# Kernel optimization log

Measured on AMD Instinct MI355X. Metric: run time of the kernel, lower is better.

Reference implementation:

```python
import jax, jax.numpy as jnp
import numpy as np

EMBED_DIM = 1024
NUM_HEADS = 16
HEAD_DIM = EMBED_DIM // NUM_HEADS
SCALE = HEAD_DIM ** -0.5
B, S = 4, 2048


def setup_inputs() -> dict:
    key = jax.random.key(0)
    ks = jax.random.split(key, 11)
    std = EMBED_DIM ** -0.5
    return {
        "query": jax.random.normal(ks[0], (B, S, EMBED_DIM), jnp.float32),
        "key": jax.random.normal(ks[1], (B, S, EMBED_DIM), jnp.float32),
        "value": jax.random.normal(ks[2], (B, S, EMBED_DIM), jnp.float32),
        "Wq": jax.random.normal(ks[3], (EMBED_DIM, EMBED_DIM), jnp.float32) * std,
        "bq": jax.random.normal(ks[4], (EMBED_DIM,), jnp.float32) * 0.01,
        "Wk": jax.random.normal(ks[5], (EMBED_DIM, EMBED_DIM), jnp.float32) * std,
        "bk": jax.random.normal(ks[6], (EMBED_DIM,), jnp.float32) * 0.01,
        "Wv": jax.random.normal(ks[7], (EMBED_DIM, EMBED_DIM), jnp.float32) * std,
        "bv": jax.random.normal(ks[8], (EMBED_DIM,), jnp.float32) * 0.01,
        "Wo": jax.random.normal(ks[9], (EMBED_DIM, EMBED_DIM), jnp.float32) * std,
        "bo": jax.random.normal(ks[10], (EMBED_DIM,), jnp.float32) * 0.01,
    }


def reference(query, key, value, Wq, bq, Wk, bk, Wv, bv, Wo, bo):
    b, s, _ = query.shape
    # torch.nn.Linear: x @ W.T + b
    q = query @ Wq.T + bq
    k = key @ Wk.T + bk
    v = value @ Wv.T + bv
    # [b, h, s, d]
    q = q.reshape(b, s, NUM_HEADS, HEAD_DIM).transpose(0, 2, 1, 3)
    k = k.reshape(b, s, NUM_HEADS, HEAD_DIM).transpose(0, 2, 1, 3)
    v = v.reshape(b, s, NUM_HEADS, HEAD_DIM).transpose(0, 2, 1, 3)
    # explicit scores [b, h, s, s]
    scores = jnp.einsum("bhqd,bhkd->bhqk", q, k) * SCALE
    causal = jnp.tril(jnp.ones((s, s), dtype=bool))  # is_causal=True
    scores = jnp.where(causal, scores, -jnp.inf)
    attn = jax.nn.softmax(scores, axis=-1)
    out = jnp.einsum("bhqk,bhkd->bhqd", attn, v)
    out = out.transpose(0, 2, 1, 3).reshape(b, s, EMBED_DIM)
    return out @ Wo.T + bo
```

## Files before the change

kernel.cpp:

```cpp
#include <hip/hip_runtime.h>


#define E 1024
#define HEADS 16
#define HD 64
#define SEQ 2048
#define BATCH 4
#define MROWS (BATCH * SEQ)

typedef __bf16 bf16x8 __attribute__((ext_vector_type(8)));
typedef __bf16 bf16x2 __attribute__((ext_vector_type(2)));
typedef float f32x4 __attribute__((ext_vector_type(4)));
typedef unsigned short ushort8v __attribute__((ext_vector_type(8)));

typedef __attribute__((address_space(1))) void gvoid;
typedef __attribute__((address_space(3))) void lvoid;

__device__ __forceinline__ void async16(const void* g, void* l) {
  __builtin_amdgcn_global_load_lds((gvoid*)g, (lvoid*)l, 16, 0, 0);
}

__device__ __forceinline__ unsigned short f2bf(float f) {
  union { float f; unsigned int u; } v;
  v.f = f;
  unsigned int r = v.u + 0x7FFFu + ((v.u >> 16) & 1u);
  return (unsigned short)(r >> 16);
}

__device__ __forceinline__ unsigned packbf(float a, float b) {
  bf16x2 t;
  t[0] = (__bf16)a;
  t[1] = (__bf16)b;
  return __builtin_bit_cast(unsigned, t);
}

__device__ __forceinline__ void store_out(unsigned short* p, float v) { *p = f2bf(v); }
__device__ __forceinline__ void store_out(float* p, float v) { *p = v; }

struct CastArgs {
  const float* src[4];
  unsigned short* dst[4];
  int n;
};

__global__ __launch_bounds__(256) void cast_kernel(CastArgs a) {
  const float* s = a.src[blockIdx.z];
  unsigned short* d = a.dst[blockIdx.z];
  const int n = a.n;
  const int stride = gridDim.x * blockDim.x * 4;
  for (int i = (blockIdx.x * blockDim.x + threadIdx.x) * 4; i < n; i += stride) {
    float4 v = *(const float4*)(s + i);
    ushort4 o;
    o.x = f2bf(v.x); o.y = f2bf(v.y); o.z = f2bf(v.z); o.w = f2bf(v.w);
    *(ushort4*)(d + i) = o;
  }
}

template <typename OutT>
__device__ __forceinline__ void gemm_body(const unsigned short* __restrict__ A,
                                          const unsigned short* __restrict__ W,
                                          const float* __restrict__ bias,
                                          OutT* __restrict__ out, float scale) {
  __shared__ unsigned short At[128 * 64];
  __shared__ unsigned short Wt[128 * 64];
  const int tid = threadIdx.x;
  const int lane = tid & 63;
  const int wv = tid >> 6;
  const int wm = wv & 1, wn = wv >> 1;
  const int li = lane & 15, g = lane >> 4;
  const int m0 = blockIdx.x * 128, n0 = blockIdx.y * 128;
  f32x4 acc[4][4] = {};

  for (int k0 = 0; k0 < E; k0 += 64) {
    __syncthreads();
#pragma unroll
    for (int i = 0; i < 4; ++i) {
      int c = tid + 256 * i;
      int row = c >> 3, slot = c & 7;
      int gc = slot ^ (row & 7);
      async16(A + (size_t)(m0 + row) * E + k0 + gc * 8, &At[c * 8]);
      async16(W + (size_t)(n0 + row) * E + k0 + gc * 8, &Wt[c * 8]);
    }
    asm volatile("s_waitcnt vmcnt(0)" ::: "memory");
    __syncthreads();
#pragma unroll
    for (int kk = 0; kk < 2; ++kk) {
      bf16x8 af[4], bfr[4];
#pragma unroll
      for (int mt = 0; mt < 4; ++mt) {
        int r = wm * 64 + mt * 16 + li;
        int slot = (kk * 4 + g) ^ (r & 7);
        af[mt] = *(const bf16x8*)&At[r * 64 + slot * 8];
      }
#pragma unroll
      for (int nt = 0; nt < 4; ++nt) {
        int r = wn * 64 + nt * 16 + li;
        int slot = (kk * 4 + g) ^ (r & 7);
        bfr[nt] = *(const bf16x8*)&Wt[r * 64 + slot * 8];
      }
#pragma unroll
      for (int mt = 0; mt < 4; ++mt)
#pragma unroll
        for (int nt = 0; nt < 4; ++nt)
          acc[mt][nt] =
              __builtin_amdgcn_mfma_f32_16x16x32_bf16(af[mt], bfr[nt], acc[mt][nt], 0, 0, 0);
    }
  }

#pragma unroll
  for (int nt = 0; nt < 4; ++nt) {
    int col = n0 + wn * 64 + nt * 16 + li;
    float bv = bias[col];
#pragma unroll
    for (int mt = 0; mt < 4; ++mt) {
#pragma unroll
      for (int r = 0; r < 4; ++r) {
        int row = m0 + wm * 64 + mt * 16 + g * 4 + r;
        store_out(&out[(size_t)row * E + col], (acc[mt][nt][r] + bv) * scale);
      }
    }
  }
}

struct QkvArgs {
  const unsigned short* A[3];
  const unsigned short* W[3];
  const float* bias[3];
  unsigned short* out[3];
  float scale[3];
};

__global__ __launch_bounds__(256) void gemm_qkv(QkvArgs p) {
  const int z = blockIdx.z;
  gemm_body<unsigned short>(p.A[z], p.W[z], p.bias[z], p.out[z], p.scale[z]);
}

__global__ __launch_bounds__(256) void gemm_out_k(const unsigned short* __restrict__ A,
                                                  const unsigned short* __restrict__ W,
                                                  const float* __restrict__ bias,
                                                  float* __restrict__ out) {
  gemm_body<float>(A, W, bias, out, 1.0f);
}

__global__ __launch_bounds__(256, 2) void flash_kernel(const unsigned short* __restrict__ Qb,
                                                       const unsigned short* __restrict__ Kb,
                                                       const unsigned short* __restrict__ Vb,
                                                       unsigned short* __restrict__ Ob) {
  __shared__ unsigned short Kt[2][128 * 64];
  __shared__ unsigned short Vt[2][64 * 128];
  const int p = blockIdx.x;
  const int bh = blockIdx.y;
  const int b = bh >> 4, h16 = bh & 15;
  const size_t base = (size_t)b * SEQ * E + (size_t)h16 * HD;
  const unsigned short* Qp = Qb + base;
  const unsigned short* Kp = Kb + base;
  const unsigned short* Vp = Vb + base;
  unsigned short* Op = Ob + base;
  const int tid = threadIdx.x, lane = tid & 63, wv = tid >> 6;
  const int li = lane & 15, g = lane >> 4;
  const int qlo = p, qhi = 15 - p;
  const int slo = ((g & 1) << 5) | li;

  bf16x8 qfL[2][2], qfH[2][2];
#pragma unroll
  for (int mt = 0; mt < 2; ++mt)
#pragma unroll
    for (int kk = 0; kk < 2; ++kk) {
      int rl = qlo * 128 + wv * 32 + mt * 16 + li;
      int rh = qhi * 128 + wv * 32 + mt * 16 + li;
      qfL[mt][kk] = *(const bf16x8*)(Qp + (size_t)rl * E + kk * 32 + g * 8);
      qfH[mt][kk] = *(const bf16x8*)(Qp + (size_t)rh * E + kk * 32 + g * 8);
    }

  f32x4 oaL[4][2] = {}, oaH[4][2] = {};
  float miL[2] = {-1e30f, -1e30f}, lsL[2] = {0.0f, 0.0f};
  float miH[2] = {-1e30f, -1e30f}, lsH[2] = {0.0f, 0.0f};

  ushort8v vv[4];

  auto loadV = [&](int j) {
#pragma unroll
    for (int i = 0; i < 4; ++i) {
      int c = tid + 256 * i;
      int key = c & 127, db = (c >> 7) * 8;
      vv[i] = *(const ushort8v*)(Vp + (size_t)(j * 128 + key) * E + db);
    }
  };
  auto stageK = [&](int j, int buf) {
#pragma unroll
    for (int i = 0; i < 4; ++i) {
      int c = tid + 256 * i;
      int row = c >> 3, slot = c & 7;
      int gc = slot ^ (row & 7);
      async16(Kp + (size_t)(j * 128 + row) * E + gc * 8, &Kt[buf][c * 8]);
    }
  };
  auto scatV = [&](int buf) {
#pragma unroll
    for (int i = 0; i < 4; ++i) {
      int c = tid + 256 * i;
      int key = c & 127, db = (c >> 7) * 8;
#pragma unroll
      for (int jj = 0; jj < 8; ++jj) {
        int n = db + jj;
        int slot = (key >> 3) ^ (n & 15);
        Vt[buf][n * 128 + slot * 8 + (key & 7)] = vv[i][jj];
      }
    }
  };

  auto compute = [&](const bf16x8 (&qf)[2][2], float (&mi)[2], float (&ls)[2],
                     f32x4 (&oa)[4][2], bool diag, int buf) {
#pragma unroll
    for (int h = 0; h < 2; ++h) {
      if (diag && h * 64 > wv * 32 + 31) continue;

      f32x4 sacc[4][2] = {};
#pragma unroll
      for (int kk = 0; kk < 2; ++kk) {
        bf16x8 kf[4];
#pragma unroll
        for (int nt = 0; nt < 4; ++nt) {
          int key = h * 64 + nt * 16 + li;
          int slot = (kk * 4 + g) ^ (key & 7);
          kf[nt] = *(const bf16x8*)&Kt[buf][key * 64 + slot * 8];
        }
#pragma unroll
        for (int nt = 0; nt < 4; ++nt)
#pragma unroll
          for (int mt = 0; mt < 2; ++mt)
            sacc[nt][mt] =
                __builtin_amdgcn_mfma_f32_16x16x32_bf16(kf[nt], qf[mt][kk], sacc[nt][mt], 0, 0, 0);
      }

      if (diag && h * 64 + 63 > wv * 32) {
#pragma unroll
        for (int nt = 0; nt < 4; ++nt)
#pragma unroll
          for (int mt = 0; mt < 2; ++mt)
#pragma unroll
            for (int r = 0; r < 4; ++r) {
              int keyg = h * 64 + nt * 16 + g * 4 + r;
              int qg = wv * 32 + mt * 16 + li;
              sacc[nt][mt][r] = (keyg > qg) ? -1e30f : sacc[nt][mt][r];
            }
      }

      float alpha[2];
#pragma unroll
      for (int mt = 0; mt < 2; ++mt) {
        float mx = sacc[0][mt][0];
#pragma unroll
        for (int nt = 0; nt < 4; ++nt)
#pragma unroll
          for (int r = 0; r < 4; ++r) mx = fmaxf(mx, sacc[nt][mt][r]);
        mx = fmaxf(mx, __shfl_xor(mx, 16));
        mx = fmaxf(mx, __shfl_xor(mx, 32));
        float mnew = fmaxf(mi[mt], mx);
        alpha[mt] = __expf(mi[mt] - mnew);
        mi[mt] = mnew;
      }

      unsigned pk[4][2][2];
      float rs[2] = {0.0f, 0.0f};
#pragma unroll
      for (int nt = 0; nt < 4; ++nt)
#pragma unroll
        for (int mt = 0; mt < 2; ++mt) {
          float p0 = __expf(sacc[nt][mt][0] - mi[mt]);
          float p1 = __expf(sacc[nt][mt][1] - mi[mt]);
          float p2 = __expf(sacc[nt][mt][2] - mi[mt]);
          float p3 = __expf(sacc[nt][mt][3] - mi[mt]);
          rs[mt] += (p0 + p1) + (p2 + p3);
          pk[nt][mt][0] = packbf(p0, p1);
          pk[nt][mt][1] = packbf(p2, p3);
        }
#pragma unroll
      for (int mt = 0; mt < 2; ++mt) {
        float s = rs[mt];
        s += __shfl_xor(s, 16);
        s += __shfl_xor(s, 32);
        ls[mt] = ls[mt] * alpha[mt] + s;
#pragma unroll
        for (int dt = 0; dt < 4; ++dt) oa[dt][mt] *= alpha[mt];
      }

#pragma unroll
      for (int kk2 = 0; kk2 < 2; ++kk2) {
        const int kc = h * 2 + kk2;
        bf16x8 vf[4];
#pragma unroll
        for (int dt = 0; dt < 4; ++dt) {
          int d = dt * 16 + li;
          int slot = (kc * 4 + g) ^ (d & 15);
          vf[dt] = *(const bf16x8*)&Vt[buf][d * 128 + slot * 8];
        }
#pragma unroll
        for (int mt = 0; mt < 2; ++mt) {
          int a0 = __shfl((int)pk[kk2 * 2][mt][0], slo);
          int a1 = __shfl((int)pk[kk2 * 2][mt][1], slo);
          int a2 = __shfl((int)pk[kk2 * 2][mt][0], slo + 16);
          int a3 = __shfl((int)pk[kk2 * 2][mt][1], slo + 16);
          int c0 = __shfl((int)pk[kk2 * 2 + 1][mt][0], slo);
          int c1 = __shfl((int)pk[kk2 * 2 + 1][mt][1], slo);
          int c2 = __shfl((int)pk[kk2 * 2 + 1][mt][0], slo + 16);
          int c3 = __shfl((int)pk[kk2 * 2 + 1][mt][1], slo + 16);
          bool hi = (g & 2) != 0;
          uint4 bb;
          bb.x = hi ? c0 : a0;
          bb.y = hi ? c1 : a1;
          bb.z = hi ? c2 : a2;
          bb.w = hi ? c3 : a3;
          bf16x8 pf = __builtin_bit_cast(bf16x8, bb);
#pragma unroll
          for (int dt = 0; dt < 4; ++dt)
            oa[dt][mt] =
                __builtin_amdgcn_mfma_f32_16x16x32_bf16(vf[dt], pf, oa[dt][mt], 0, 0, 0);
        }
      }
    }
  };

  loadV(0);
  stageK(0, 0);
  scatV(0);

  for (int j = 0; j <= qhi; ++j) {
    const int buf = j & 1;
    asm volatile("s_waitcnt vmcnt(0)" ::: "memory");
    __syncthreads();
    if (j < qhi) {
      loadV(j + 1);
      stageK(j + 1, buf ^ 1);
    }
    compute(qfH, miH, lsH, oaH, j == qhi, buf);
    if (j <= qlo) compute(qfL, miL, lsL, oaL, j == qlo, buf);
    if (j < qhi) scatV(buf ^ 1);
  }

#pragma unroll
  for (int t = 0; t < 2; ++t) {
    const int qt = t ? qhi : qlo;
    f32x4(&oa)[4][2] = t ? oaH : oaL;
    float* ls = t ? lsH : lsL;
#pragma unroll
    for (int mt = 0; mt < 2; ++mt) {
      float inv = 1.0f / ls[mt];
      int row = qt * 128 + wv * 32 + mt * 16 + li;
#pragma unroll
      for (int dt = 0; dt < 4; ++dt) {
        ushort4 w;
        w.x = f2bf(oa[dt][mt][0] * inv);
        w.y = f2bf(oa[dt][mt][1] * inv);
        w.z = f2bf(oa[dt][mt][2] * inv);
        w.w = f2bf(oa[dt][mt][3] * inv);
        *(ushort4*)(Op + (size_t)row * E + dt * 16 + g * 4) = w;
      }
    }
  }
}

extern "C" void kernel_launch(void* const* d_in, const int* in_sizes, int n_in,
                              void* d_out, int out_size, void* d_ws, size_t ws_size,
                              hipStream_t stream) {
  const float* q  = (const float*)d_in[0];
  const float* k  = (const float*)d_in[1];
  const float* v  = (const float*)d_in[2];
  const float* Wq = (const float*)d_in[3];
  const float* bq = (const float*)d_in[4];
  const float* Wk = (const float*)d_in[5];
  const float* bk = (const float*)d_in[6];
  const float* Wv = (const float*)d_in[7];
  const float* bv = (const float*)d_in[8];
  const float* Wo = (const float*)d_in[9];
  const float* bo = (const float*)d_in[10];

  unsigned short* Xq  = (unsigned short*)d_ws;
  unsigned short* Xk  = Xq + (size_t)MROWS * E;
  unsigned short* Xv  = Xk + (size_t)MROWS * E;
  unsigned short* Wqb = Xv + (size_t)MROWS * E;
  unsigned short* Wkb = Wqb + (size_t)E * E;
  unsigned short* Wvb = Wkb + (size_t)E * E;
  unsigned short* Wob = Wvb + (size_t)E * E;
  unsigned short* Qb  = Wob + (size_t)E * E;
  unsigned short* Kb  = Qb + (size_t)MROWS * E;
  unsigned short* Vb  = Kb + (size_t)MROWS * E;
  unsigned short* Og  = Xq;

  CastArgs ca;
  ca.src[0] = q; ca.src[1] = k; ca.src[2] = v; ca.src[3] = nullptr;
  ca.dst[0] = Xq; ca.dst[1] = Xk; ca.dst[2] = Xv; ca.dst[3] = nullptr;
  ca.n = MROWS * E;
  cast_kernel<<<dim3(1024, 1, 3), 256, 0, stream>>>(ca);

  CastArgs cw;
  cw.src[0] = Wq; cw.src[1] = Wk; cw.src[2] = Wv; cw.src[3] = Wo;
  cw.dst[0] = Wqb; cw.dst[1] = Wkb; cw.dst[2] = Wvb; cw.dst[3] = Wob;
  cw.n = E * E;
  cast_kernel<<<dim3(256, 1, 4), 256, 0, stream>>>(cw);

  QkvArgs p;
  p.A[0] = Xq;  p.A[1] = Xk;  p.A[2] = Xv;
  p.W[0] = Wqb; p.W[1] = Wkb; p.W[2] = Wvb;
  p.bias[0] = bq; p.bias[1] = bk; p.bias[2] = bv;
  p.out[0] = Qb; p.out[1] = Kb; p.out[2] = Vb;
  p.scale[0] = 0.125f; p.scale[1] = 1.0f; p.scale[2] = 1.0f;
  gemm_qkv<<<dim3(64, 8, 3), 256, 0, stream>>>(p);

  flash_kernel<<<dim3(8, 64), 256, 0, stream>>>(Qb, Kb, Vb, Og);

  gemm_out_k<<<dim3(64, 8), 256, 0, stream>>>(Og, Wob, bo, (float*)d_out);
}
```

Before: 405.7 us.

## Single-buffer V tile, use 16x16x16 MFMA for PV without shuffles, merge casts

The PV product now uses the 16x16x16 bf16 MFMA, so the packed probability fragments feed the instruction directly and the per-tile cross-lane shuffles go away. V goes from a double buffer to a single LDS buffer, scattered at the start of each iteration behind an extra barrier, which cuts LDS use and allows launch bounds of 3 blocks per CU. The two cast launches are merged into one 7-slice launch, and bf16 packing switches to the manual rounding helper. In exchange, the V transpose scatter no longer overlaps compute, there is an extra __syncthreads per iteration, and twice as many MFMA instructions are issued for the PV product.

```diff
diff --git a/kernel.cpp b/kernel.cpp
--- a/kernel.cpp
+++ b/kernel.cpp
@@ -9,8 +9,8 @@
 #define MROWS (BATCH * SEQ)
 
 typedef __bf16 bf16x8 __attribute__((ext_vector_type(8)));
-typedef __bf16 bf16x2 __attribute__((ext_vector_type(2)));
 typedef float f32x4 __attribute__((ext_vector_type(4)));
+typedef short s16x4 __attribute__((ext_vector_type(4)));
 typedef unsigned short ushort8v __attribute__((ext_vector_type(8)));
 
 typedef __attribute__((address_space(1))) void gvoid;
@@ -27,26 +27,19 @@
   return (unsigned short)(r >> 16);
 }
 
-__device__ __forceinline__ unsigned packbf(float a, float b) {
-  bf16x2 t;
-  t[0] = (__bf16)a;
-  t[1] = (__bf16)b;
-  return __builtin_bit_cast(unsigned, t);
-}
-
 __device__ __forceinline__ void store_out(unsigned short* p, float v) { *p = f2bf(v); }
 __device__ __forceinline__ void store_out(float* p, float v) { *p = v; }
 
 struct CastArgs {
-  const float* src[4];
-  unsigned short* dst[4];
-  int n;
+  const float* src[7];
+  unsigned short* dst[7];
+  int n[7];
 };
 
 __global__ __launch_bounds__(256) void cast_kernel(CastArgs a) {
   const float* s = a.src[blockIdx.z];
   unsigned short* d = a.dst[blockIdx.z];
-  const int n = a.n;
+  const int n = a.n[blockIdx.z];
   const int stride = gridDim.x * blockDim.x * 4;
   for (int i = (blockIdx.x * blockDim.x + threadIdx.x) * 4; i < n; i += stride) {
     float4 v = *(const float4*)(s + i);
@@ -142,12 +135,12 @@
   gemm_body<float>(A, W, bias, out, 1.0f);
 }
 
-__global__ __launch_bounds__(256, 2) void flash_kernel(const unsigned short* __restrict__ Qb,
+__global__ __launch_bounds__(256, 3) void flash_kernel(const unsigned short* __restrict__ Qb,
                                                        const unsigned short* __restrict__ Kb,
                                                        const unsigned short* __restrict__ Vb,
                                                        unsigned short* __restrict__ Ob) {
   __shared__ unsigned short Kt[2][128 * 64];
-  __shared__ unsigned short Vt[2][64 * 128];
+  __shared__ unsigned short Vt[64 * 128];
   const int p = blockIdx.x;
   const int bh = blockIdx.y;
   const int b = bh >> 4, h16 = bh & 15;
@@ -159,7 +152,6 @@
   const int tid = threadIdx.x, lane = tid & 63, wv = tid >> 6;
   const int li = lane & 15, g = lane >> 4;
   const int qlo = p, qhi = 15 - p;
-  const int slo = ((g & 1) << 5) | li;
 
   bf16x8 qfL[2][2], qfH[2][2];
 #pragma unroll
@@ -195,7 +187,7 @@
       async16(Kp + (size_t)(j * 128 + row) * E + gc * 8, &Kt[buf][c * 8]);
     }
   };
-  auto scatV = [&](int buf) {
+  auto scatV = [&]() {
 #pragma unroll
     for (int i = 0; i < 4; ++i) {
       int c = tid + 256 * i;
@@ -204,7 +196,7 @@
       for (int jj = 0; jj < 8; ++jj) {
         int n = db + jj;
         int slot = (key >> 3) ^ (n & 15);
-        Vt[buf][n * 128 + slot * 8 + (key & 7)] = vv[i][jj];
+        Vt[n * 128 + slot * 8 + (key & 7)] = vv[i][jj];
       }
     }
   };
@@ -261,7 +253,7 @@
         mi[mt] = mnew;
       }
 
-      unsigned pk[4][2][2];
+      s16x4 pk[4][2];
       float rs[2] = {0.0f, 0.0f};
 #pragma unroll
       for (int nt = 0; nt < 4; ++nt)
@@ -272,8 +264,12 @@
           float p2 = __expf(sacc[nt][mt][2] - mi[mt]);
           float p3 = __expf(sacc[nt][mt][3] - mi[mt]);
           rs[mt] += (p0 + p1) + (p2 + p3);
-          pk[nt][mt][0] = packbf(p0, p1);
-          pk[nt][mt][1] = packbf(p2, p3);
+          s16x4 t;
+          t[0] = (short)f2bf(p0);
+          t[1] = (short)f2bf(p1);
+          t[2] = (short)f2bf(p2);
+          t[3] = (short)f2bf(p3);
+          pk[nt][mt] = t;
         }
 #pragma unroll
       for (int mt = 0; mt < 2; ++mt) {
@@ -286,56 +282,40 @@
       }
 
 #pragma unroll
-      for (int kk2 = 0; kk2 < 2; ++kk2) {
-        const int kc = h * 2 + kk2;
-        bf16x8 vf[4];
+      for (int nt = 0; nt < 4; ++nt) {
+        s16x4 va[4];
 #pragma unroll
         for (int dt = 0; dt < 4; ++dt) {
           int d = dt * 16 + li;
-          int slot = (kc * 4 + g) ^ (d & 15);
-          vf[dt] = *(const bf16x8*)&Vt[buf][d * 128 + slot * 8];
+          int K0 = h * 64 + nt * 16 + g * 4;
+          int slot = (K0 >> 3) ^ (d & 15);
+          va[dt] = *(const s16x4*)&Vt[d * 128 + slot * 8 + (K0 & 7)];
         }
 #pragma unroll
-        for (int mt = 0; mt < 2; ++mt) {
-          int a0 = __shfl((int)pk[kk2 * 2][mt][0], slo);
-          int a1 = __shfl((int)pk[kk2 * 2][mt][1], slo);
-          int a2 = __shfl((int)pk[kk2 * 2][mt][0], slo + 16);
-          int a3 = __shfl((int)pk[kk2 * 2][mt][1], slo + 16);
-          int c0 = __shfl((int)pk[kk2 * 2 + 1][mt][0], slo);
-          int c1 = __shfl((int)pk[kk2 * 2 + 1][mt][1], slo);
-          int c2 = __shfl((int)pk[kk2 * 2 + 1][mt][0], slo + 16);
-          int c3 = __shfl((int)pk[kk2 * 2 + 1][mt][1], slo + 16);
-          bool hi = (g & 2) != 0;
-          uint4 bb;
-          bb.x = hi ? c0 : a0;
-          bb.y = hi ? c1 : a1;
-          bb.z = hi ? c2 : a2;
-          bb.w = hi ? c3 : a3;
-          bf16x8 pf = __builtin_bit_cast(bf16x8, bb);
+        for (int mt = 0; mt < 2; ++mt)
 #pragma unroll
           for (int dt = 0; dt < 4; ++dt)
-            oa[dt][mt] =
-                __builtin_amdgcn_mfma_f32_16x16x32_bf16(vf[dt], pf, oa[dt][mt], 0, 0, 0);
-        }
+            oa[dt][mt] = __builtin_amdgcn_mfma_f32_16x16x16bf16_1k(va[dt], pk[nt][mt],
+                                                                   oa[dt][mt], 0, 0, 0);
       }
     }
   };
 
   loadV(0);
   stageK(0, 0);
-  scatV(0);
 
   for (int j = 0; j <= qhi; ++j) {
     const int buf = j & 1;
     asm volatile("s_waitcnt vmcnt(0)" ::: "memory");
     __syncthreads();
+    scatV();
+    __syncthreads();
     if (j < qhi) {
       loadV(j + 1);
       stageK(j + 1, buf ^ 1);
     }
     compute(qfH, miH, lsH, oaH, j == qhi, buf);
     if (j <= qlo) compute(qfL, miL, lsL, oaL, j == qlo, buf);
-    if (j < qhi) scatV(buf ^ 1);
   }
 
 #pragma unroll
@@ -388,16 +368,14 @@
   unsigned short* Og  = Xq;
 
   CastArgs ca;
-  ca.src[0] = q; ca.src[1] = k; ca.src[2] = v; ca.src[3] = nullptr;
-  ca.dst[0] = Xq; ca.dst[1] = Xk; ca.dst[2] = Xv; ca.dst[3] = nullptr;
-  ca.n = MROWS * E;
-  cast_kernel<<<dim3(1024, 1, 3), 256, 0, stream>>>(ca);
-
-  CastArgs cw;
-  cw.src[0] = Wq; cw.src[1] = Wk; cw.src[2] = Wv; cw.src[3] = Wo;
-  cw.dst[0] = Wqb; cw.dst[1] = Wkb; cw.dst[2] = Wvb; cw.dst[3] = Wob;
-  cw.n = E * E;
-  cast_kernel<<<dim3(256, 1, 4), 256, 0, stream>>>(cw);
+  ca.src[0] = q;  ca.dst[0] = Xq;  ca.n[0] = MROWS * E;
+  ca.src[1] = k;  ca.dst[1] = Xk;  ca.n[1] = MROWS * E;
+  ca.src[2] = v;  ca.dst[2] = Xv;  ca.n[2] = MROWS * E;
+  ca.src[3] = Wq; ca.dst[3] = Wqb; ca.n[3] = E * E;
+  ca.src[4] = Wk; ca.dst[4] = Wkb; ca.n[4] = E * E;
+  ca.src[5] = Wv; ca.dst[5] = Wvb; ca.n[5] = E * E;
+  ca.src[6] = Wo; ca.dst[6] = Wob; ca.n[6] = E * E;
+  cast_kernel<<<dim3(512, 1, 7), 256, 0, stream>>>(ca);
 
   QkvArgs p;
   p.A[0] = Xq;  p.A[1] = Xk;  p.A[2] = Xv;
```

After: 549.4 us. +35.4%, slower.
